# Kernel tuning notes

Measured on AMD Instinct MI355X. Metric: run time of the kernel, lower is better.

The kernel has to match this reference:

```python
import jax, jax.numpy as jnp
import numpy as np

GAMMA = 0.2
B, C, K = 2048, 32000, 8
BIG = 1e8


def setup_inputs() -> dict:
    key = jax.random.key(0)
    k1, k2, k3 = jax.random.split(key, 3)
    x = jax.random.normal(k1, (B, C), dtype=jnp.float32)
    y = jax.random.randint(k2, (B, K), 0, C, dtype=jnp.int32)
    neg = jax.random.uniform(k3, (B, K)) < 0.3
    neg = neg.at[:, 0].set(False)
    y = jnp.where(neg, jnp.int32(-1), y)
    return {"x": x, "y": y}


def _forward(x, y):
    Bn, Cn = x.shape
    target = y[:, 0]
    # loss1: standard mean cross-entropy on primary label
    logp = jax.nn.log_softmax(x, axis=1)
    loss1 = -jnp.mean(jnp.take_along_axis(logp, target[:, None].astype(jnp.int32), axis=1))
    pos_mask = y != -1                                   # [B, K]
    sample_mask = jnp.sum(pos_mask, axis=1) > 1          # rows with >1 positive label
    y_safe = jnp.where(pos_mask, y, 0)
    # gather logits at all positive labels; padding slots get +BIG so argmin/min ignores them
    pos_data = jnp.where(pos_mask, jnp.take_along_axis(x, y_safe, axis=1), BIG)
    min_rel = jnp.min(pos_data, axis=1, keepdims=True)   # [B, 1] = min positive logit
    # scatter -BIG into x at every positive label position (padding scatters add 0 at col 0)
    row = jnp.arange(Bn, dtype=jnp.int32)[:, None]
    hit = jnp.zeros((Bn, Cn), jnp.int32).at[row, y_safe].add(pos_mask.astype(jnp.int32))
    new_x = jnp.where(hit > 0, -BIG, x)                  # positives suppressed
    # relative CE: min positive logit (class 0) vs. all non-positive logits
    rel = jnp.concatenate([min_rel, new_x], axis=1)      # [B, C+1]
    ce2 = -jax.nn.log_softmax(rel, axis=1)[:, 0]
    cnt = jnp.sum(sample_mask.astype(x.dtype))
    loss2 = jnp.sum(jnp.where(sample_mask, ce2, jnp.zeros_like(ce2))) / jnp.maximum(cnt, 1.0)
    return loss1 + GAMMA * loss2


def reference(x, y):
    return _forward(x, y)
```

## Files before the change

### kernel.cpp

```cpp
#include <hip/hip_runtime.h>
#include <math.h>

#define GAMMA 0.2f
#define BN 2048
#define CN 32000
#define KN 8
#define BIGV 100000000.0f

__global__ __launch_bounds__(256) void row_kernel(const float* __restrict__ x,
                                                  const int* __restrict__ y,
                                                  float4* __restrict__ row_out) {
    const int row = blockIdx.x;
    const int tid = threadIdx.x;
    const float* xrow = x + (size_t)row * CN;
    const float4* xr = reinterpret_cast<const float4*>(xrow);

    int yv[KN];
    float xv[KN];
    if (tid == 0) {
        #pragma unroll
        for (int k = 0; k < KN; ++k) yv[k] = y[row * KN + k];
        #pragma unroll
        for (int k = 0; k < KN; ++k) xv[k] = xrow[yv[k] == -1 ? 0 : yv[k]];
    }

    float s0 = 0.f, s1 = 0.f, s2 = 0.f, s3 = 0.f;
    #pragma unroll
    for (int it = 0; it < 28; it += 4) {
        float4 a = xr[tid + (it + 0) * 256];
        float4 b = xr[tid + (it + 1) * 256];
        float4 c = xr[tid + (it + 2) * 256];
        float4 d = xr[tid + (it + 3) * 256];
        s0 += (__expf(a.x) + __expf(a.y)) + (__expf(a.z) + __expf(a.w));
        s1 += (__expf(b.x) + __expf(b.y)) + (__expf(b.z) + __expf(b.w));
        s2 += (__expf(c.x) + __expf(c.y)) + (__expf(c.z) + __expf(c.w));
        s3 += (__expf(d.x) + __expf(d.y)) + (__expf(d.z) + __expf(d.w));
    }
    #pragma unroll
    for (int it = 28; it < 31; ++it) {
        float4 a = xr[tid + it * 256];
        s0 += (__expf(a.x) + __expf(a.y)) + (__expf(a.z) + __expf(a.w));
    }
    if (tid < 64) {
        float4 a = xr[tid + 31 * 256];
        s1 += (__expf(a.x) + __expf(a.y)) + (__expf(a.z) + __expf(a.w));
    }
    float s = (s0 + s1) + (s2 + s3);

    #pragma unroll
    for (int off = 1; off < 64; off <<= 1) s += __shfl_xor(s, off);

    __shared__ float ss[4];
    const int wave = tid >> 6;
    if ((tid & 63) == 0) ss[wave] = s;
    __syncthreads();

    if (tid == 0) {
        const float S = (ss[0] + ss[1]) + (ss[2] + ss[3]);
        const float lse = logf(S);
        const float loss1 = lse - xv[0];

        int npos = 0;
        float min_rel = BIGV;
        float sum_hit = 0.f;
        #pragma unroll
        for (int k = 0; k < KN; ++k) {
            if (yv[k] != -1) {
                ++npos;
                min_rel = fminf(min_rel, xv[k]);
                bool dup = false;
                for (int j = 0; j < k; ++j) dup = dup || (yv[j] == yv[k]);
                if (!dup) sum_hit += __expf(xv[k]);
            }
        }
        float ce2 = 0.f, msk = 0.f;
        if (npos > 1) {
            const float rest = fmaxf(S - sum_hit, 0.f);
            ce2 = logf(__expf(min_rel) + rest) - min_rel;
            msk = 1.f;
        }
        row_out[row] = make_float4(loss1, ce2, msk, 0.f);
    }
}

__global__ __launch_bounds__(256) void finalize_kernel(const float4* __restrict__ row_out,
                                                       float* __restrict__ out) {
    const int tid = threadIdx.x;
    float s1 = 0.f, s2 = 0.f, sc = 0.f;
    for (int i = tid; i < BN; i += 256) {
        const float4 v = row_out[i];
        s1 += v.x; s2 += v.y; sc += v.z;
    }
    #pragma unroll
    for (int off = 1; off < 64; off <<= 1) {
        s1 += __shfl_xor(s1, off);
        s2 += __shfl_xor(s2, off);
        sc += __shfl_xor(sc, off);
    }
    __shared__ float a1[4], a2[4], ac[4];
    const int wave = tid >> 6;
    if ((tid & 63) == 0) { a1[wave] = s1; a2[wave] = s2; ac[wave] = sc; }
    __syncthreads();
    if (tid == 0) {
        #pragma unroll
        for (int w = 1; w < 4; ++w) { s1 += a1[w]; s2 += a2[w]; sc += ac[w]; }
        out[0] = s1 / (float)BN + GAMMA * (s2 / fmaxf(sc, 1.0f));
    }
}

extern "C" void kernel_launch(void* const* d_in, const int* in_sizes, int n_in,
                              void* d_out, int out_size, void* d_ws, size_t ws_size,
                              hipStream_t stream) {
    const float* x = (const float*)d_in[0];
    const int* y = (const int*)d_in[1];
    float4* row_out = (float4*)d_ws;

    row_kernel<<<BN, 256, 0, stream>>>(x, y, row_out);
    finalize_kernel<<<1, 256, 0, stream>>>(row_out, (float*)d_out);
}
```

Before: 48.21 us.

## Fuse finalize into row kernel via last-block atomic counter, use nontemporal loads

Merges the separate finalize launch into the row kernel: each block publishes its per-row partials, bumps a global atomic counter, and the last block to finish does the final reduction. The label gather is spread over 8 threads through shared memory instead of being done serially by thread 0. Streaming loads of x become nontemporal. It also adds a memset launch to reset the counter, plus fences and an extra barrier in every block.

```diff
diff --git a/kernel.cpp b/kernel.cpp
--- a/kernel.cpp
+++ b/kernel.cpp
@@ -7,70 +7,78 @@
 #define KN 8
 #define BIGV 100000000.0f
 
-__global__ __launch_bounds__(256) void row_kernel(const float* __restrict__ x,
-                                                  const int* __restrict__ y,
-                                                  float4* __restrict__ row_out) {
+typedef float fx4 __attribute__((ext_vector_type(4)));
+
+__global__ __launch_bounds__(256) void fused_kernel(const float* __restrict__ x,
+                                                    const int* __restrict__ y,
+                                                    float4* __restrict__ row_out,
+                                                    unsigned int* __restrict__ counter,
+                                                    float* __restrict__ out) {
     const int row = blockIdx.x;
     const int tid = threadIdx.x;
     const float* xrow = x + (size_t)row * CN;
-    const float4* xr = reinterpret_cast<const float4*>(xrow);
+    const fx4* xr = (const fx4*)xrow;
 
-    int yv[KN];
-    float xv[KN];
-    if (tid == 0) {
-        #pragma unroll
-        for (int k = 0; k < KN; ++k) yv[k] = y[row * KN + k];
-        #pragma unroll
-        for (int k = 0; k < KN; ++k) xv[k] = xrow[yv[k] == -1 ? 0 : yv[k]];
+    __shared__ int s_y[KN];
+    __shared__ float s_xv[KN];
+    __shared__ float ss[4];
+    __shared__ bool s_last;
+
+    if (tid < KN) {
+        const int yk = y[row * KN + tid];
+        s_y[tid] = yk;
+        s_xv[tid] = xrow[yk == -1 ? 0 : yk];
     }
 
     float s0 = 0.f, s1 = 0.f, s2 = 0.f, s3 = 0.f;
     #pragma unroll
     for (int it = 0; it < 28; it += 4) {
-        float4 a = xr[tid + (it + 0) * 256];
-        float4 b = xr[tid + (it + 1) * 256];
-        float4 c = xr[tid + (it + 2) * 256];
-        float4 d = xr[tid + (it + 3) * 256];
-        s0 += (__expf(a.x) + __expf(a.y)) + (__expf(a.z) + __expf(a.w));
-        s1 += (__expf(b.x) + __expf(b.y)) + (__expf(b.z) + __expf(b.w));
-        s2 += (__expf(c.x) + __expf(c.y)) + (__expf(c.z) + __expf(c.w));
-        s3 += (__expf(d.x) + __expf(d.y)) + (__expf(d.z) + __expf(d.w));
+        fx4 a = __builtin_nontemporal_load(&xr[tid + (it + 0) * 256]);
+        fx4 b = __builtin_nontemporal_load(&xr[tid + (it + 1) * 256]);
+        fx4 c = __builtin_nontemporal_load(&xr[tid + (it + 2) * 256]);
+        fx4 d = __builtin_nontemporal_load(&xr[tid + (it + 3) * 256]);
+        s0 += (__expf(a[0]) + __expf(a[1])) + (__expf(a[2]) + __expf(a[3]));
+        s1 += (__expf(b[0]) + __expf(b[1])) + (__expf(b[2]) + __expf(b[3]));
+        s2 += (__expf(c[0]) + __expf(c[1])) + (__expf(c[2]) + __expf(c[3]));
+        s3 += (__expf(d[0]) + __expf(d[1])) + (__expf(d[2]) + __expf(d[3]));
     }
     #pragma unroll
     for (int it = 28; it < 31; ++it) {
-        float4 a = xr[tid + it * 256];
-        s0 += (__expf(a.x) + __expf(a.y)) + (__expf(a.z) + __expf(a.w));
+        fx4 a = __builtin_nontemporal_load(&xr[tid + it * 256]);
+        s0 += (__expf(a[0]) + __expf(a[1])) + (__expf(a[2]) + __expf(a[3]));
     }
     if (tid < 64) {
-        float4 a = xr[tid + 31 * 256];
-        s1 += (__expf(a.x) + __expf(a.y)) + (__expf(a.z) + __expf(a.w));
+        fx4 a = __builtin_nontemporal_load(&xr[tid + 31 * 256]);
+        s1 += (__expf(a[0]) + __expf(a[1])) + (__expf(a[2]) + __expf(a[3]));
     }
     float s = (s0 + s1) + (s2 + s3);
 
     #pragma unroll
     for (int off = 1; off < 64; off <<= 1) s += __shfl_xor(s, off);
 
-    __shared__ float ss[4];
     const int wave = tid >> 6;
     if ((tid & 63) == 0) ss[wave] = s;
     __syncthreads();
 
     if (tid == 0) {
         const float S = (ss[0] + ss[1]) + (ss[2] + ss[3]);
-        const float lse = logf(S);
-        const float loss1 = lse - xv[0];
+        const float loss1 = logf(S) - s_xv[0];
 
         int npos = 0;
         float min_rel = BIGV;
         float sum_hit = 0.f;
+        int yv[KN];
+        #pragma unroll
+        for (int k = 0; k < KN; ++k) yv[k] = s_y[k];
         #pragma unroll
         for (int k = 0; k < KN; ++k) {
             if (yv[k] != -1) {
                 ++npos;
-                min_rel = fminf(min_rel, xv[k]);
+                const float xv = s_xv[k];
+                min_rel = fminf(min_rel, xv);
                 bool dup = false;
                 for (int j = 0; j < k; ++j) dup = dup || (yv[j] == yv[k]);
-                if (!dup) sum_hit += __expf(xv[k]);
+                if (!dup) sum_hit += __expf(xv);
             }
         }
         float ce2 = 0.f, msk = 0.f;
@@ -80,31 +88,33 @@
             msk = 1.f;
         }
         row_out[row] = make_float4(loss1, ce2, msk, 0.f);
+        __threadfence();
+        const unsigned int old = atomicAdd(counter, 1u);
+        s_last = (old == BN - 1);
     }
-}
+    __syncthreads();
 
-__global__ __launch_bounds__(256) void finalize_kernel(const float4* __restrict__ row_out,
-                                                       float* __restrict__ out) {
-    const int tid = threadIdx.x;
-    float s1 = 0.f, s2 = 0.f, sc = 0.f;
-    for (int i = tid; i < BN; i += 256) {
-        const float4 v = row_out[i];
-        s1 += v.x; s2 += v.y; sc += v.z;
-    }
-    #pragma unroll
-    for (int off = 1; off < 64; off <<= 1) {
-        s1 += __shfl_xor(s1, off);
-        s2 += __shfl_xor(s2, off);
-        sc += __shfl_xor(sc, off);
-    }
-    __shared__ float a1[4], a2[4], ac[4];
-    const int wave = tid >> 6;
-    if ((tid & 63) == 0) { a1[wave] = s1; a2[wave] = s2; ac[wave] = sc; }
-    __syncthreads();
-    if (tid == 0) {
+    if (s_last) {
+        __threadfence();
+        float r1 = 0.f, r2 = 0.f, rc = 0.f;
+        for (int i = tid; i < BN; i += 256) {
+            const float4 v = row_out[i];
+            r1 += v.x; r2 += v.y; rc += v.z;
+        }
         #pragma unroll
-        for (int w = 1; w < 4; ++w) { s1 += a1[w]; s2 += a2[w]; sc += ac[w]; }
-        out[0] = s1 / (float)BN + GAMMA * (s2 / fmaxf(sc, 1.0f));
+        for (int off = 1; off < 64; off <<= 1) {
+            r1 += __shfl_xor(r1, off);
+            r2 += __shfl_xor(r2, off);
+            rc += __shfl_xor(rc, off);
+        }
+        __shared__ float a1[4], a2[4], ac[4];
+        if ((tid & 63) == 0) { a1[wave] = r1; a2[wave] = r2; ac[wave] = rc; }
+        __syncthreads();
+        if (tid == 0) {
+            #pragma unroll
+            for (int w = 1; w < 4; ++w) { r1 += a1[w]; r2 += a2[w]; rc += ac[w]; }
+            out[0] = r1 / (float)BN + GAMMA * (r2 / fmaxf(rc, 1.0f));
+        }
     }
 }
 
@@ -114,7 +124,8 @@
     const float* x = (const float*)d_in[0];
     const int* y = (const int*)d_in[1];
     float4* row_out = (float4*)d_ws;
+    unsigned int* counter = (unsigned int*)((char*)d_ws + BN * sizeof(float4));
 
-    row_kernel<<<BN, 256, 0, stream>>>(x, y, row_out);
-    finalize_kernel<<<1, 256, 0, stream>>>(row_out, (float*)d_out);
+    hipMemsetAsync(counter, 0, sizeof(unsigned int), stream);
+    fused_kernel<<<BN, 256, 0, stream>>>(x, y, row_out, counter, (float*)d_out);
 }
```

Measured after the change: 151.1 us. 213% more time.

## Process two rows per block and parallelize label gathers across threads

Applied to the files above, without the earlier changes.

Each block now handles two rows, interleaving their loads and exp-sums, and the grid shrinks to half as many blocks. The eight label gathers per row are spread over 16 threads through shared memory instead of being done serially by thread 0, which shortens the per-row tail. This puts more memory requests in flight per thread but halves the number of blocks, which may reduce how many rows are processed concurrently across the GPU.

```diff
diff --git a/kernel.cpp b/kernel.cpp
--- a/kernel.cpp
+++ b/kernel.cpp
@@ -7,58 +7,76 @@
 #define KN 8
 #define BIGV 100000000.0f
 
+typedef float fx4 __attribute__((ext_vector_type(4)));
+
+#define EXP4(v) ((__expf((v)[0]) + __expf((v)[1])) + (__expf((v)[2]) + __expf((v)[3])))
+
 __global__ __launch_bounds__(256) void row_kernel(const float* __restrict__ x,
                                                   const int* __restrict__ y,
                                                   float4* __restrict__ row_out) {
-    const int row = blockIdx.x;
+    const int blk = blockIdx.x;
     const int tid = threadIdx.x;
-    const float* xrow = x + (size_t)row * CN;
-    const float4* xr = reinterpret_cast<const float4*>(xrow);
+    const int r0 = 2 * blk;
+    const float* xrow0 = x + (size_t)r0 * CN;
+    const float* xrow1 = xrow0 + CN;
+    const fx4* xr0 = (const fx4*)xrow0;
+    const fx4* xr1 = (const fx4*)xrow1;
 
-    int yv[KN];
-    float xv[KN];
-    if (tid == 0) {
-        #pragma unroll
-        for (int k = 0; k < KN; ++k) yv[k] = y[row * KN + k];
-        #pragma unroll
-        for (int k = 0; k < KN; ++k) xv[k] = xrow[yv[k] == -1 ? 0 : yv[k]];
+    __shared__ int s_y[2][KN];
+    __shared__ float s_xv[2][KN];
+    __shared__ float ss[4][2];
+
+    if (tid < 2 * KN) {
+        const int r = tid >> 3, k = tid & 7;
+        const int yk = y[(r0 + r) * KN + k];
+        s_y[r][k] = yk;
+        s_xv[r][k] = x[(size_t)(r0 + r) * CN + (yk == -1 ? 0 : yk)];
     }
 
-    float s0 = 0.f, s1 = 0.f, s2 = 0.f, s3 = 0.f;
+    float a0 = 0.f, a1 = 0.f, b0 = 0.f, b1 = 0.f;
     #pragma unroll
-    for (int it = 0; it < 28; it += 4) {
-        float4 a = xr[tid + (it + 0) * 256];
-        float4 b = xr[tid + (it + 1) * 256];
-        float4 c = xr[tid + (it + 2) * 256];
-        float4 d = xr[tid + (it + 3) * 256];
-        s0 += (__expf(a.x) + __expf(a.y)) + (__expf(a.z) + __expf(a.w));
-        s1 += (__expf(b.x) + __expf(b.y)) + (__expf(b.z) + __expf(b.w));
-        s2 += (__expf(c.x) + __expf(c.y)) + (__expf(c.z) + __expf(c.w));
-        s3 += (__expf(d.x) + __expf(d.y)) + (__expf(d.z) + __expf(d.w));
+    for (int it = 0; it < 28; it += 2) {
+        fx4 p = xr0[tid + (it + 0) * 256];
+        fx4 q = xr1[tid + (it + 0) * 256];
+        fx4 r = xr0[tid + (it + 1) * 256];
+        fx4 t = xr1[tid + (it + 1) * 256];
+        a0 += EXP4(p);
+        b0 += EXP4(q);
+        a1 += EXP4(r);
+        b1 += EXP4(t);
     }
     #pragma unroll
     for (int it = 28; it < 31; ++it) {
-        float4 a = xr[tid + it * 256];
-        s0 += (__expf(a.x) + __expf(a.y)) + (__expf(a.z) + __expf(a.w));
+        fx4 p = xr0[tid + it * 256];
+        fx4 q = xr1[tid + it * 256];
+        a0 += EXP4(p);
+        b0 += EXP4(q);
     }
     if (tid < 64) {
-        float4 a = xr[tid + 31 * 256];
-        s1 += (__expf(a.x) + __expf(a.y)) + (__expf(a.z) + __expf(a.w));
+        fx4 p = xr0[tid + 31 * 256];
+        fx4 q = xr1[tid + 31 * 256];
+        a1 += EXP4(p);
+        b1 += EXP4(q);
     }
-    float s = (s0 + s1) + (s2 + s3);
+    float sa = a0 + a1;
+    float sb = b0 + b1;
 
     #pragma unroll
-    for (int off = 1; off < 64; off <<= 1) s += __shfl_xor(s, off);
-
-    __shared__ float ss[4];
+    for (int off = 1; off < 64; off <<= 1) {
+        sa += __shfl_xor(sa, off);
+        sb += __shfl_xor(sb, off);
+    }
     const int wave = tid >> 6;
-    if ((tid & 63) == 0) ss[wave] = s;
+    if ((tid & 63) == 0) { ss[wave][0] = sa; ss[wave][1] = sb; }
     __syncthreads();
 
-    if (tid == 0) {
-        const float S = (ss[0] + ss[1]) + (ss[2] + ss[3]);
-        const float lse = logf(S);
-        const float loss1 = lse - xv[0];
+    if (tid < 2) {
+        const float S = (ss[0][tid] + ss[1][tid]) + (ss[2][tid] + ss[3][tid]);
+        const float loss1 = logf(S) - s_xv[tid][0];
+
+        int yv[KN];
+        #pragma unroll
+        for (int k = 0; k < KN; ++k) yv[k] = s_y[tid][k];
 
         int npos = 0;
         float min_rel = BIGV;
@@ -67,10 +85,11 @@
         for (int k = 0; k < KN; ++k) {
             if (yv[k] != -1) {
                 ++npos;
-                min_rel = fminf(min_rel, xv[k]);
+                const float xv = s_xv[tid][k];
+                min_rel = fminf(min_rel, xv);
                 bool dup = false;
                 for (int j = 0; j < k; ++j) dup = dup || (yv[j] == yv[k]);
-                if (!dup) sum_hit += __expf(xv[k]);
+                if (!dup) sum_hit += __expf(xv);
             }
         }
         float ce2 = 0.f, msk = 0.f;
@@ -79,7 +98,7 @@
             ce2 = logf(__expf(min_rel) + rest) - min_rel;
             msk = 1.f;
         }
-        row_out[row] = make_float4(loss1, ce2, msk, 0.f);
+        row_out[r0 + tid] = make_float4(loss1, ce2, msk, 0.f);
     }
 }
 
@@ -115,6 +134,6 @@
     const int* y = (const int*)d_in[1];
     float4* row_out = (float4*)d_ws;
 
-    row_kernel<<<BN, 256, 0, stream>>>(x, y, row_out);
+    row_kernel<<<BN / 2, 256, 0, stream>>>(x, y, row_out);
     finalize_kernel<<<1, 256, 0, stream>>>(row_out, (float*)d_out);
 }
```

After: 48.84 us. No clear change (+1.3%).
